# Kernel tuning notes

Hardware: AMD Instinct MI355X
Metric: run time of the kernel (lower is better)

The kernel has to match this reference:

```python
import jax, jax.numpy as jnp
import numpy as np

H, W = 256, 256
DX, DY = 1.0, 1.0
EI, KC, GC = 1.0, 1.0, 1.0
LAYERS = [2, 256, 512, 1024, H * W]
B = 64


def _d2x(f, dx):
    # reflect-pad width 1 on x (last axis), stencil [1, -2, 1]
    p = jnp.pad(f, ((0, 0), (0, 0), (0, 0), (1, 1)), mode='reflect')
    return (p[..., :-2] - 2.0 * p[..., 1:-1] + p[..., 2:]) / (dx * dx)


def _d2y(f, dy):
    p = jnp.pad(f, ((0, 0), (0, 0), (1, 1), (0, 0)), mode='reflect')
    return (p[:, :, :-2, :] - 2.0 * p[:, :, 1:-1, :] + p[:, :, 2:, :]) / (dy * dy)


def setup_inputs() -> dict:
    key = jax.random.key(0)
    ks = jax.random.split(key, 10)
    inp = {
        'x_coloc': jax.random.normal(ks[0], (B, LAYERS[0]), jnp.float32),
        'P': jax.random.normal(ks[1], (B, H * W), jnp.float32),
    }
    for i in range(4):
        inp[f'W{i + 1}'] = jax.random.normal(ks[2 + i], (LAYERS[i], LAYERS[i + 1]), jnp.float32) / np.sqrt(LAYERS[i]).astype(np.float32)
        inp[f'b{i + 1}'] = jnp.zeros((LAYERS[i + 1],), jnp.float32)
    return inp


def reference(x_coloc, P, W1, b1, W2, b2, W3, b3, W4, b4):
    # MLP field predictor: Linear+ReLU x3, final Linear -> [B, H*W]
    h = jax.nn.relu(x_coloc @ W1 + b1)
    h = jax.nn.relu(h @ W2 + b2)
    h = jax.nn.relu(h @ W3 + b3)
    f = h @ W4 + b4                      # [B, H*W]
    fm = f.reshape(B, 1, H, W)

    fx2 = _d2x(fm, DX)                   # d2/dx2
    fy2 = _d2y(fm, DY)                   # d2/dy2
    lap = fx2 + fy2
    biharmonic = _d2x(lap, DX) + _d2y(lap, DY)

    residual = EI * biharmonic + GC * (fx2 + fy2) + KC * fm - P.reshape(B, 1, H, W)
    return residual.reshape(B, H * W)
```

## Files before the change

### kernel.cpp

```cpp
#include <hip/hip_runtime.h>


#define BATCH 64
#define NPIX 65536

typedef __attribute__((ext_vector_type(8))) short short8_t;
typedef __attribute__((ext_vector_type(4))) float f32x4;

__device__ __forceinline__ short f2bf(float x) {
    unsigned u = __float_as_uint(x);
    unsigned r = (u + 0x7fffu + ((u >> 16) & 1u)) >> 16;
    return (short)r;
}

__global__ void k_layer12(const float* __restrict__ x, const float* __restrict__ W1,
                          const float* __restrict__ b1, const float* __restrict__ W2,
                          const float* __restrict__ b2, float* __restrict__ h2) {
    __shared__ float As[16][64];
    __shared__ float Ws[64][16];
    int tid = threadIdx.x;
    int tn = tid & 15, tm = tid >> 4;
    int n0 = blockIdx.x * 16, m0 = blockIdx.y * 16;
    float acc = 0.f;
    for (int k0 = 0; k0 < 256; k0 += 64) {
#pragma unroll
        for (int j = 0; j < 4; ++j) {
            int e = j * 256 + tid;
            int m = m0 + (e >> 6), kk = k0 + (e & 63);
            float v = x[m * 2 + 0] * W1[kk] + x[m * 2 + 1] * W1[256 + kk] + b1[kk];
            As[e >> 6][e & 63] = v > 0.f ? v : 0.f;
        }
#pragma unroll
        for (int j = 0; j < 4; ++j) {
            int e = j * 256 + tid;
            Ws[e >> 4][e & 15] = W2[(k0 + (e >> 4)) * 512 + n0 + (e & 15)];
        }
        __syncthreads();
#pragma unroll
        for (int k = 0; k < 64; ++k)
            acc += As[tm][k] * Ws[k][tn];
        __syncthreads();
    }
    acc += b2[n0 + tn];
    acc = acc > 0.f ? acc : 0.f;
    h2[(m0 + tm) * 512 + n0 + tn] = acc;
}

__global__ void k_layer3(const float* __restrict__ A, const float* __restrict__ Wt,
                         const float* __restrict__ bias, short* __restrict__ out_bf) {
    __shared__ float As[16][64];
    __shared__ float Ws[64][16];
    int tid = threadIdx.x;
    int tn = tid & 15, tm = tid >> 4;
    int n0 = blockIdx.x * 16, m0 = blockIdx.y * 16;
    float acc = 0.f;
    for (int k0 = 0; k0 < 512; k0 += 64) {
#pragma unroll
        for (int j = 0; j < 4; ++j) {
            int e = j * 256 + tid;
            As[e >> 6][e & 63] = A[(m0 + (e >> 6)) * 512 + k0 + (e & 63)];
        }
#pragma unroll
        for (int j = 0; j < 4; ++j) {
            int e = j * 256 + tid;
            Ws[e >> 4][e & 15] = Wt[(k0 + (e >> 4)) * 1024 + n0 + (e & 15)];
        }
        __syncthreads();
#pragma unroll
        for (int k = 0; k < 64; ++k)
            acc += As[tm][k] * Ws[k][tn];
        __syncthreads();
    }
    acc += bias[n0 + tn];
    acc = acc > 0.f ? acc : 0.f;
    out_bf[(m0 + tm) * 1024 + n0 + tn] = f2bf(acc);
}

__global__ __launch_bounds__(256) void k_gemm_mfma(
        const short* __restrict__ A,
        const float* __restrict__ W,
        const float* __restrict__ bias,
        float* __restrict__ f) {
    __shared__ float Wt[2][32 * 128];
    __shared__ short At[2][4 * 64 * 8];
    const int tid = threadIdx.x;
    const int w = tid >> 6;
    const int lane = tid & 63;
    const int lr = lane & 15;
    const int g = lane >> 4;
    const int n0 = blockIdx.x * 128;

    f32x4 acc[4][2];
#pragma unroll
    for (int a = 0; a < 4; ++a)
#pragma unroll
        for (int b = 0; b < 2; ++b)
            acc[a][b] = {0.f, 0.f, 0.f, 0.f};

    auto stage = [&](int b, int s) {
#pragma unroll
        for (int i = 0; i < 4; ++i) {
            int c = i * 256 + tid;
            int k = c >> 5;
            int q4 = (c & 31) * 4;
            int csw = q4 ^ (((k >> 3) & 1) << 4);
            const float* src = W + (size_t)(s * 32 + k) * NPIX + n0 + csw;
            __builtin_amdgcn_global_load_lds(
                (const __attribute__((address_space(1))) void*)src,
                (__attribute__((address_space(3))) void*)((char*)&Wt[b][0] + c * 16),
                16, 0, 0);
        }
        {
            int kq = tid >> 6;
            int ms = tid & 63;
            int md = ms ^ (kq << 2);
            const short* asrc = A + md * 1024 + s * 32 + kq * 8;
            __builtin_amdgcn_global_load_lds(
                (const __attribute__((address_space(1))) void*)asrc,
                (__attribute__((address_space(3))) void*)((char*)&At[b][0] + tid * 16),
                16, 0, 0);
        }
    };

    stage(0, 0);

    for (int s = 0; s < 32; ++s) {
        const int cur = s & 1;
        if (s < 31) {
            stage(cur ^ 1, s + 1);
            asm volatile("s_waitcnt vmcnt(5)" ::: "memory");
        } else {
            asm volatile("s_waitcnt vmcnt(0)" ::: "memory");
        }
        __builtin_amdgcn_sched_barrier(0);
        __builtin_amdgcn_s_barrier();

        short8_t afr[4];
#pragma unroll
        for (int mt = 0; mt < 4; ++mt) {
            int mrow = mt * 16 + lr;
            afr[mt] = *(const short8_t*)((const short*)&At[cur][0] +
                                         g * 512 + (mrow ^ (g << 2)) * 8);
        }
#pragma unroll
        for (int t = 0; t < 2; ++t) {
            const int col = w * 32 + t * 16 + lr;
            const int csw = col ^ ((g & 1) << 4);
            short8_t bfr;
#pragma unroll
            for (int j = 0; j < 8; ++j)
                bfr[j] = f2bf(Wt[cur][(g * 8 + j) * 128 + csw]);
#pragma unroll
            for (int mt = 0; mt < 4; ++mt)
                acc[mt][t] = __builtin_amdgcn_mfma_f32_16x16x32_bf16(afr[mt], bfr, acc[mt][t], 0, 0, 0);
        }
        __builtin_amdgcn_s_barrier();
    }

#pragma unroll
    for (int t = 0; t < 2; ++t) {
        const int col = n0 + w * 32 + t * 16 + lr;
        float bb = bias[col];
#pragma unroll
        for (int mt = 0; mt < 4; ++mt) {
            int rowb = mt * 16 + g * 4;
#pragma unroll
            for (int r = 0; r < 4; ++r)
                f[(size_t)(rowb + r) * NPIX + col] = acc[mt][t][r] + bb;
        }
    }
}

#define ROWS 16
__device__ __forceinline__ int rfl(int i) {
    return i < 0 ? -i : (i > 255 ? 510 - i : i);
}
__global__ void k_stencil(const float* __restrict__ f, const float* __restrict__ P,
                          float* __restrict__ out) {
    __shared__ float fs[ROWS + 4][256];
    int x = threadIdx.x;
    int y0 = blockIdx.x * ROWS;
    int b = blockIdx.y;
    const float* fb = f + (size_t)b * NPIX;
    for (int t = 0; t < ROWS + 4; ++t) {
        int gy = rfl(y0 - 2 + t);
        fs[t][x] = fb[gy * 256 + x];
    }
    __syncthreads();

    int xm = x == 0 ? 1 : x - 1;
    int xp = x == 255 ? 254 : x + 1;

    auto lapAt = [&](int j, int i) {
        int s = j - y0 + 2;
        int sm = rfl(j - 1) - y0 + 2;
        int sp = rfl(j + 1) - y0 + 2;
        int im = i == 0 ? 1 : i - 1;
        int ip = i == 255 ? 254 : i + 1;
        float c = fs[s][i];
        return (fs[sm][i] - 2.f * c + fs[sp][i]) + (fs[s][im] - 2.f * c + fs[s][ip]);
    };

    for (int r = 0; r < ROWS; ++r) {
        int y = y0 + r;
        float lc = lapAt(y, x);
        float lym = lapAt(rfl(y - 1), x);
        float lyp = lapAt(rfl(y + 1), x);
        float lxm = lapAt(y, xm);
        float lxp = lapAt(y, xp);
        float bih = (lym - 2.f * lc + lyp) + (lxm - 2.f * lc + lxp);
        float fc = fs[r + 2][x];
        size_t idx = (size_t)b * NPIX + y * 256 + x;
        out[idx] = bih + lc + fc - P[idx];
    }
}

extern "C" void kernel_launch(void* const* d_in, const int* in_sizes, int n_in,
                              void* d_out, int out_size, void* d_ws, size_t ws_size,
                              hipStream_t stream) {
    const float* x  = (const float*)d_in[0];
    const float* P  = (const float*)d_in[1];
    const float* W1 = (const float*)d_in[2];
    const float* b1 = (const float*)d_in[3];
    const float* W2 = (const float*)d_in[4];
    const float* b2 = (const float*)d_in[5];
    const float* W3 = (const float*)d_in[6];
    const float* b3 = (const float*)d_in[7];
    const float* W4 = (const float*)d_in[8];
    const float* b4 = (const float*)d_in[9];
    float* out = (float*)d_out;

    char* ws = (char*)d_ws;
    float* h2  = (float*)(ws);
    short* h3b = (short*)(ws + (128 << 10));
    float* f   = (float*)(ws + (256 << 10));

    k_layer12<<<dim3(512 / 16, 4), 256, 0, stream>>>(x, W1, b1, W2, b2, h2);
    k_layer3<<<dim3(1024 / 16, 4), 256, 0, stream>>>(h2, W3, b3, h3b);
    k_gemm_mfma<<<NPIX / 128, 256, 0, stream>>>(h3b, W4, b4, f);
    k_stencil<<<dim3(256 / ROWS, BATCH), 256, 0, stream>>>(f, P, out);
}
```

Before: 87.39 us.

## Stage GEMM epilogue through LDS and precompute Laplacian rows in stencil

The GEMM epilogue now writes accumulators into LDS (reusing the W tile buffer) and then stores them to global memory as coalesced 16-byte vectors, replacing scattered scalar stores. The stencil kernel computes each Laplacian value once into a shared ls buffer instead of recomputing it five times per output pixel, which removes redundant LDS reads and ALU work. It also switches to the HIP bf16 conversion intrinsic and adds a sched barrier. In exchange there are extra __syncthreads calls and more shared memory per block.

```diff
diff --git a/kernel.cpp b/kernel.cpp
--- a/kernel.cpp
+++ b/kernel.cpp
@@ -1,4 +1,5 @@
 #include <hip/hip_runtime.h>
+#include <hip/hip_bf16.h>
 
 
 #define BATCH 64
@@ -8,9 +9,10 @@
 typedef __attribute__((ext_vector_type(4))) float f32x4;
 
 __device__ __forceinline__ short f2bf(float x) {
-    unsigned u = __float_as_uint(x);
-    unsigned r = (u + 0x7fffu + ((u >> 16) & 1u)) >> 16;
-    return (short)r;
+    __hip_bfloat16 h = __float2bfloat16(x);
+    short s;
+    __builtin_memcpy(&s, &h, 2);
+    return s;
 }
 
 __global__ void k_layer12(const float* __restrict__ x, const float* __restrict__ W1,
@@ -134,6 +136,7 @@
         }
         __builtin_amdgcn_sched_barrier(0);
         __builtin_amdgcn_s_barrier();
+        __builtin_amdgcn_sched_barrier(0);
 
         short8_t afr[4];
 #pragma unroll
@@ -157,17 +160,25 @@
         __builtin_amdgcn_s_barrier();
     }
 
+    __syncthreads();
+    float* Cl = (float*)&Wt[0][0];
 #pragma unroll
     for (int t = 0; t < 2; ++t) {
-        const int col = n0 + w * 32 + t * 16 + lr;
-        float bb = bias[col];
-#pragma unroll
-        for (int mt = 0; mt < 4; ++mt) {
-            int rowb = mt * 16 + g * 4;
+        const int colb = w * 32 + t * 16 + lr;
+        float bb = bias[n0 + colb];
+#pragma unroll
+        for (int mt = 0; mt < 4; ++mt)
 #pragma unroll
             for (int r = 0; r < 4; ++r)
-                f[(size_t)(rowb + r) * NPIX + col] = acc[mt][t][r] + bb;
-        }
+                Cl[(mt * 16 + g * 4 + r) * 128 + colb] = acc[mt][t][r] + bb;
+    }
+    __syncthreads();
+#pragma unroll
+    for (int it = 0; it < 8; ++it) {
+        int row = (tid >> 5) + it * 8;
+        int cc = (tid & 31) * 4;
+        f32x4 v = *(const f32x4*)&Cl[row * 128 + cc];
+        *(f32x4*)(f + (size_t)row * NPIX + n0 + cc) = v;
     }
 }
 
@@ -178,10 +189,12 @@
 __global__ void k_stencil(const float* __restrict__ f, const float* __restrict__ P,
                           float* __restrict__ out) {
     __shared__ float fs[ROWS + 4][256];
+    __shared__ float ls[ROWS + 2][256];
     int x = threadIdx.x;
     int y0 = blockIdx.x * ROWS;
     int b = blockIdx.y;
     const float* fb = f + (size_t)b * NPIX;
+#pragma unroll
     for (int t = 0; t < ROWS + 4; ++t) {
         int gy = rfl(y0 - 2 + t);
         fs[t][x] = fb[gy * 256 + x];
@@ -191,24 +204,24 @@
     int xm = x == 0 ? 1 : x - 1;
     int xp = x == 255 ? 254 : x + 1;
 
-    auto lapAt = [&](int j, int i) {
-        int s = j - y0 + 2;
-        int sm = rfl(j - 1) - y0 + 2;
-        int sp = rfl(j + 1) - y0 + 2;
-        int im = i == 0 ? 1 : i - 1;
-        int ip = i == 255 ? 254 : i + 1;
-        float c = fs[s][i];
-        return (fs[sm][i] - 2.f * c + fs[sp][i]) + (fs[s][im] - 2.f * c + fs[s][ip]);
-    };
-
+#pragma unroll
+    for (int t = 0; t < ROWS + 2; ++t) {
+        int jj = rfl(y0 - 1 + t);
+        int s  = jj - y0 + 2;
+        int sm = rfl(jj - 1) - y0 + 2;
+        int sp = rfl(jj + 1) - y0 + 2;
+        float c = fs[s][x];
+        ls[t][x] = (fs[sm][x] - 2.f * c + fs[sp][x]) +
+                   (fs[s][xm] - 2.f * c + fs[s][xp]);
+    }
+    __syncthreads();
+
+#pragma unroll
     for (int r = 0; r < ROWS; ++r) {
         int y = y0 + r;
-        float lc = lapAt(y, x);
-        float lym = lapAt(rfl(y - 1), x);
-        float lyp = lapAt(rfl(y + 1), x);
-        float lxm = lapAt(y, xm);
-        float lxp = lapAt(y, xp);
-        float bih = (lym - 2.f * lc + lyp) + (lxm - 2.f * lc + lxp);
+        float lc = ls[r + 1][x];
+        float bih = (ls[r][x] - 2.f * lc + ls[r + 2][x]) +
+                    (ls[r + 1][xm] - 2.f * lc + ls[r + 1][xp]);
         float fc = fs[r + 2][x];
         size_t idx = (size_t)b * NPIX + y * 256 + x;
         out[idx] = bih + lc + fc - P[idx];
```

Result: faster. 81.97 us (-6.2%).
